# Performance work log

Measured on AMD Instinct MI355X. Metric: run time of the kernel, lower is better.

The kernel has to match this reference:

```python
import jax, jax.numpy as jnp
import numpy as np

N_NODES = 20000
N_EDGES = 320000
F_IN = 64      # num_node_features
C = 64         # out_features (per-head channels, concat=False)
H = 4          # n_heads
L = 3          # n_layers (stackable since F_IN == C)
N_RES = 2
N_PAIRS = 8192
EDGE_DIM = 9
HID = 64 * C   # ResNetGated hidden dim = 64 * out_features
N_EXPERTS = 8


def setup_inputs() -> dict:
    key = jax.random.key(0)
    ks = jax.random.split(key, 24)
    s = 0.05
    f32 = jnp.float32
    inp = {}
    inp["x"] = jax.random.normal(ks[0], (N_NODES, F_IN), f32)
    inp["edge_index"] = jax.random.randint(ks[1], (2, N_EDGES), 0, N_NODES)
    inp["edge_attr"] = jax.random.normal(ks[2], (N_EDGES, EDGE_DIM), f32)
    inp["edge_cross"] = jax.random.randint(ks[3], (N_PAIRS, 2), 0, N_NODES)
    inp["types"] = jax.random.randint(ks[4], (N_PAIRS,), 0, N_EXPERTS)
    # GATv2 encoder params, stacked over L layers (layer 0 in-dim == C)
    inp["gat_Wl"] = jax.random.normal(ks[5], (L, F_IN, H * C), f32) * s
    inp["gat_bl"] = jnp.full((L, H * C), 0.01, f32)
    inp["gat_Wr"] = jax.random.normal(ks[6], (L, F_IN, H * C), f32) * s
    inp["gat_br"] = jnp.full((L, H * C), 0.01, f32)
    inp["gat_We"] = jax.random.normal(ks[7], (L, EDGE_DIM, H * C), f32) * s  # lin_edge, no bias
    inp["gat_att"] = jax.random.normal(ks[8], (L, H, C), f32) * s
    inp["gat_bias"] = jnp.zeros((L, C), f32)
    inp["gat_gates"] = jax.random.normal(ks[9], (L,), f32) * 0.5
    # 8 type-routed experts: ResNetGated(2C -> 64C -> 2C) x N_RES, then Linear(2C, 1)
    inp["res_W1"] = jax.random.normal(ks[10], (N_EXPERTS, N_RES, 2 * C, HID), f32) * s
    inp["res_b1"] = jnp.full((N_EXPERTS, N_RES, HID), 0.01, f32)
    inp["res_W2"] = jax.random.normal(ks[11], (N_EXPERTS, N_RES, HID, 2 * C), f32) * s
    inp["res_b2"] = jnp.full((N_EXPERTS, N_RES, 2 * C), 0.01, f32)
    inp["res_gates"] = jax.random.normal(ks[12], (N_EXPERTS, N_RES), f32) * 0.5
    inp["head_W"] = jax.random.normal(ks[13], (N_EXPERTS, 2 * C, 1), f32) * s
    inp["head_b"] = jnp.full((N_EXPERTS, 1), 0.01, f32)
    return inp


def _gat_layer(h, src, tgt, ea, Wl, bl, Wr, br, We, att, bias):
    # GATv2Conv with edge features, concat=False (mean over heads)
    n = h.shape[0]
    nh, c = att.shape
    xl = (h @ Wl + bl).reshape(n, nh, c)   # source transform (x_j)
    xr = (h @ Wr + br).reshape(n, nh, c)   # target transform (x_i)
    e = (ea @ We).reshape(-1, nh, c)
    m = jax.nn.leaky_relu(xl[src] + xr[tgt] + e, 0.2)       # [E,H,C]
    logits = jnp.einsum('ehc,hc->eh', m, att)               # [E,H]
    mx = jax.ops.segment_max(logits, tgt, num_segments=n)
    a = jnp.exp(logits - mx[tgt])
    den = jax.ops.segment_sum(a, tgt, num_segments=n)
    alpha = a / den[tgt]                                     # segment softmax over in-edges
    out = jax.ops.segment_sum(xl[src] * alpha[:, :, None], tgt, num_segments=n)
    return out.mean(axis=1) + bias


def reference(x, edge_index, edge_attr, edge_cross, types,
              gat_Wl, gat_bl, gat_Wr, gat_br, gat_We, gat_att, gat_bias, gat_gates,
              res_W1, res_b1, res_W2, res_b2, res_gates, head_W, head_b):
    src, tgt = edge_index[0], edge_index[1]
    g = jax.nn.sigmoid(gat_gates)
    h = _gat_layer(x, src, tgt, edge_attr, gat_Wl[0], gat_bl[0], gat_Wr[0], gat_br[0],
                   gat_We[0], gat_att[0], gat_bias[0])
    for i in range(1, gat_Wl.shape[0]):
        h = jax.nn.leaky_relu(h, 0.01)
        hi = _gat_layer(h, src, tgt, edge_attr, gat_Wl[i], gat_bl[i], gat_Wr[i], gat_br[i],
                        gat_We[i], gat_att[i], gat_bias[i])
        h = g[i - 1] * hi + (1 - g[i - 1]) * h
    # pair gather + feature interleave: x[edge_cross].transpose(1,2).reshape(P, 2C)
    pair = h[edge_cross]                               # [P,2,C]
    p = pair.shape[0]
    z0 = jnp.swapaxes(pair, 1, 2).reshape(p, -1)        # [P,2C]
    outs = []
    for e in range(res_W1.shape[0]):
        z = z0
        ge = jax.nn.sigmoid(res_gates[e])
        for r in range(res_W1.shape[1]):
            z = jax.nn.relu(z)
            y = jax.nn.relu(z @ res_W1[e, r] + res_b1[e, r]) @ res_W2[e, r] + res_b2[e, r]
            z = ge[r] * y + (1 - ge[r]) * z
        outs.append(z @ head_W[e] + head_b[e])          # [P,1]
    all_out = jnp.stack(outs)                           # [8,P,1]
    per_row = all_out[types, jnp.arange(p)]             # [P,1] per-row expert output
    order = jnp.argsort(types, stable=True)             # concat groups type 0..7, stable in-group
    return per_row[order]
```

## Files before the change

kernel.cpp:

```cpp
#include <hip/hip_runtime.h>

#define NN 20000
#define NE 320000
#define NL 3
#define NP 8192
#define EDIM 9
#define TROWS 32
#define MAXT 272
#define CAPR (MAXT*TROWS)

typedef _Float16 f16x8 __attribute__((ext_vector_type(8)));
typedef float f32x4 __attribute__((ext_vector_type(4)));

#define GLL16(g,l) __builtin_amdgcn_global_load_lds((const __attribute__((address_space(1))) unsigned int*)(g), (__attribute__((address_space(3))) unsigned int*)(l), 16, 0, 0)

__device__ __forceinline__ float sigm(float x){ return 1.f/(1.f+__expf(-x)); }

__device__ __forceinline__ float dpp_sum64(float x){
  x += __int_as_float(__builtin_amdgcn_update_dpp(0, __float_as_int(x), 0x111, 0xf, 0xf, true));
  x += __int_as_float(__builtin_amdgcn_update_dpp(0, __float_as_int(x), 0x112, 0xf, 0xf, true));
  x += __int_as_float(__builtin_amdgcn_update_dpp(0, __float_as_int(x), 0x114, 0xf, 0xf, true));
  x += __int_as_float(__builtin_amdgcn_update_dpp(0, __float_as_int(x), 0x118, 0xf, 0xf, true));
  x += __int_as_float(__builtin_amdgcn_update_dpp(0, __float_as_int(x), 0x142, 0xf, 0xf, true));
  x += __int_as_float(__builtin_amdgcn_update_dpp(0, __float_as_int(x), 0x143, 0xf, 0xf, true));
  return __uint_as_float(__builtin_amdgcn_readlane(__float_as_uint(x), 63));
}

__global__ void k_fill_i(int* __restrict__ p, int n, int v){ int i=blockIdx.x*blockDim.x+threadIdx.x; if(i<n)p[i]=v; }

__global__ void k_deg(const int* __restrict__ ei, int* __restrict__ deg){
  int e=blockIdx.x*blockDim.x+threadIdx.x; if(e<NE) atomicAdd(&deg[ei[NE+e]],1);
}

__global__ __launch_bounds__(1024) void k_scan(const int* __restrict__ deg, int* __restrict__ row_ptr, int* __restrict__ cursor){
  __shared__ int sh[1024];
  __shared__ int carry;
  int tid=threadIdx.x;
  if(tid==0) carry=0;
  __syncthreads();
  for(int base=0;base<NN;base+=1024){
    int i=base+tid;
    int v=(i<NN)?deg[i]:0;
    sh[tid]=v; __syncthreads();
    for(int o=1;o<1024;o<<=1){
      int t=(tid>=o)?sh[tid-o]:0; __syncthreads();
      sh[tid]+=t; __syncthreads();
    }
    int incl=sh[tid];
    int c=carry;
    if(i<NN){ row_ptr[i+1]=c+incl; cursor[i]=c+incl-v; }
    if(i==0) row_ptr[0]=0;
    __syncthreads();
    if(tid==1023) carry=c+incl;
    __syncthreads();
  }
}

__global__ void k_fill_csr2(const int* __restrict__ ei, const float* __restrict__ ea,
    int* __restrict__ cursor, int* __restrict__ csr_src, float* __restrict__ eas){
  int e=blockIdx.x*blockDim.x+threadIdx.x;
  if(e<NE){
    int t=ei[NE+e]; int pos=atomicAdd(&cursor[t],1);
    csr_src[pos]=ei[e];
    const float* s=ea+(size_t)e*9;
    float* d=eas+(size_t)pos*12;
    #pragma unroll
    for(int k=0;k<9;++k) d[k]=s[k];
    d[9]=0.f; d[10]=0.f; d[11]=0.f;
  }
}

__global__ __launch_bounds__(256) void k_sort(const int* __restrict__ types, int* __restrict__ meta,
    int* __restrict__ slotp, int* __restrict__ islot){
  __shared__ int cnt[256][8];
  __shared__ int tot[8];
  __shared__ int base_s[8], pad_s[8];
  int tid=threadIdx.x;
  int lc[8]={0,0,0,0,0,0,0,0};
  int tl[32];
  for(int i=0;i<32;++i){ int ty=types[tid*32+i]; tl[i]=ty; lc[ty]++; }
  #pragma unroll
  for(int t=0;t<8;++t) cnt[tid][t]=lc[t];
  __syncthreads();
  if(tid<8){
    int run=0;
    for(int j=0;j<256;++j){ int v=cnt[j][tid]; cnt[j][tid]=run; run+=v; }
    tot[tid]=run;
  }
  __syncthreads();
  if(tid==0){
    int b=0, pb=0, nt=0;
    for(int t=0;t<8;++t){
      base_s[t]=b; pad_s[t]=pb;
      meta[t]=tot[t]; meta[8+t]=b; meta[16+t]=pb;
      int ntt=(tot[t]+31)>>5;
      for(int j=0;j<ntt;++j){ meta[32+nt]=t; meta[32+MAXT+nt]=pb+j*32; nt++; }
      b+=tot[t]; pb+=ntt*32;
    }
    meta[24]=nt; meta[25]=pb;
  }
  __syncthreads();
  if(tid<8){
    int t=tid; int ntt=(tot[t]+31)>>5;
    for(int sr=tot[t]; sr<ntt*32; ++sr) islot[pad_s[t]+sr]=-1;
  }
  int run[8];
  #pragma unroll
  for(int t=0;t<8;++t) run[t]=cnt[tid][t];
  for(int i=0;i<32;++i){
    int p=tid*32+i; int t=tl[i]; int r=run[t]++;
    int pos=base_s[t]+r, slot=pad_s[t]+r;
    slotp[p]=slot; islot[slot]=pos;
  }
}

__global__ __launch_bounds__(256) void k_nodexf(const float* __restrict__ hin,
    const float* __restrict__ Wl, const float* __restrict__ bl,
    const float* __restrict__ Wr, const float* __restrict__ br,
    float* __restrict__ xl, float* __restrict__ xr, int lk){
  __shared__ float hsT[64][68];
  __shared__ float ws[64][68];
  int bid=blockIdx.x;
  int n0=(bid>>3)*64, ch=bid&7;
  const float* W=(ch<4)?Wl:Wr;
  const float* bb=(ch<4)?bl:br;
  float* outp=(ch<4)?xl:xr;
  int c0=(ch&3)*64;
  int tid=threadIdx.x;

  for(int idx=tid; idx<64*16; idx+=256){
    int r=idx&63, kq=idx>>6;
    int n=n0+r;
    float4 v=make_float4(0.f,0.f,0.f,0.f);
    if(n<NN) v=*(const float4*)&hin[(size_t)n*64+kq*4];
    if(lk){
      v.x=v.x>0.f?v.x:0.01f*v.x; v.y=v.y>0.f?v.y:0.01f*v.y;
      v.z=v.z>0.f?v.z:0.01f*v.z; v.w=v.w>0.f?v.w:0.01f*v.w;
    }
    hsT[kq*4+0][r]=v.x; hsT[kq*4+1][r]=v.y; hsT[kq*4+2][r]=v.z; hsT[kq*4+3][r]=v.w;
  }
  for(int idx=tid; idx<64*16; idx+=256){
    int k=idx>>4, j4=idx&15;
    *(float4*)&ws[k][j4*4]=*(const float4*)&W[(size_t)k*256+c0+j4*4];
  }
  __syncthreads();

  int ty=tid>>4, tx=tid&15;
  float acc[4][4]={};
  #pragma unroll 4
  for(int k=0;k<64;++k){
    float4 a=*(const float4*)&hsT[k][4*ty];
    float4 b=*(const float4*)&ws[k][4*tx];
    float aa[4]={a.x,a.y,a.z,a.w}, bbv[4]={b.x,b.y,b.z,b.w};
    #pragma unroll
    for(int i=0;i<4;++i){
      #pragma unroll
      for(int j=0;j<4;++j) acc[i][j]=fmaf(aa[i],bbv[j],acc[i][j]);
    }
  }
  float4 bias4=*(const float4*)&bb[c0+4*tx];
  #pragma unroll
  for(int i=0;i<4;++i){
    int n=n0+4*ty+i;
    if(n<NN){
      float4 o=make_float4(acc[i][0]+bias4.x, acc[i][1]+bias4.y, acc[i][2]+bias4.z, acc[i][3]+bias4.w);
      *(float4*)&outp[(size_t)n*256+c0+4*tx]=o;
    }
  }
}

__global__ __launch_bounds__(256) void k_agg2(const float* __restrict__ xl, const float* __restrict__ xr,
    const float* __restrict__ eas, const int* __restrict__ csr_src, const int* __restrict__ row_ptr,
    const float* __restrict__ WeL, const float* __restrict__ attL,
    const float* __restrict__ biasL, const float* __restrict__ gates, int layer,
    const float* __restrict__ hprev, float* __restrict__ hout){
  __shared__ float red[4][64];
  int n=blockIdx.x, tid=threadIdx.x;
  float w0=WeL[tid],      w1=WeL[256+tid],  w2=WeL[512+tid],  w3=WeL[768+tid],  w4=WeL[1024+tid];
  float w5=WeL[1280+tid], w6=WeL[1536+tid], w7=WeL[1792+tid], w8=WeL[2048+tid];
  float att_t=attL[tid];
  float xr_t=xr[(size_t)n*256+tid];
  int s=row_ptr[n], t=row_ptr[n+1];
  float den=0.f, acc=0.f;

  auto body=[&](float xlv, int j){
    const float4* ep=(const float4*)(eas+(size_t)j*12);
    float4 e0=ep[0], e1=ep[1];
    float e8=eas[(size_t)j*12+8];
    float ev=e0.x*w0+e0.y*w1+e0.z*w2+e0.w*w3+e1.x*w4+e1.y*w5+e1.z*w6+e1.w*w7+e8*w8;
    float m=xlv+xr_t+ev;
    m=m>0.f?m:0.2f*m;
    float pt=dpp_sum64(m*att_t);
    float a=__expf(pt);
    den+=a; acc+=a*xlv;
  };

  float x0=0.f,x1=0.f,x2=0.f,x3=0.f;
  if(s+0<t) x0=xl[(size_t)csr_src[s+0]*256+tid];
  if(s+1<t) x1=xl[(size_t)csr_src[s+1]*256+tid];
  if(s+2<t) x2=xl[(size_t)csr_src[s+2]*256+tid];
  if(s+3<t) x3=xl[(size_t)csr_src[s+3]*256+tid];
  int j=s;
  while(j+7<t){
    float y0=xl[(size_t)csr_src[j+4]*256+tid];
    float y1=xl[(size_t)csr_src[j+5]*256+tid];
    float y2=xl[(size_t)csr_src[j+6]*256+tid];
    float y3=xl[(size_t)csr_src[j+7]*256+tid];
    body(x0,j); body(x1,j+1); body(x2,j+2); body(x3,j+3);
    x0=y0; x1=y1; x2=y2; x3=y3;
    j+=4;
  }
  if(j<t){ body(x0,j); ++j; }
  if(j<t){ body(x1,j); ++j; }
  if(j<t){ body(x2,j); ++j; }
  if(j<t){ body(x3,j); ++j; }
  while(j<t){ body(xl[(size_t)csr_src[j]*256+tid], j); ++j; }

  float rdn=den>0.f?1.f/den:0.f;
  int h=tid>>6, cc=tid&63;
  red[h][cc]=acc*rdn;
  __syncthreads();
  if(tid<64){
    float mean=(red[0][tid]+red[1][tid]+red[2][tid]+red[3][tid])*0.25f + biasL[tid];
    float o;
    if(layer==0) o=mean;
    else{
      float hp=hprev[(size_t)n*64+tid];
      hp=hp>0.f?hp:0.01f*hp;
      float g=sigm(gates[layer-1]);
      o=g*mean+(1.f-g)*hp;
    }
    hout[(size_t)n*64+tid]=o;
  }
}

__global__ void k_buildz(const float* __restrict__ hfin, const int* __restrict__ ecross,
    const int* __restrict__ slotp, float* __restrict__ z){
  int g=blockIdx.x*blockDim.x+threadIdx.x;
  if(g>=NP*64) return;
  int p=g>>6, c=g&63;
  int a=ecross[2*p], b=ecross[2*p+1];
  int slot=slotp[p];
  float2 v; v.x=hfin[(size_t)a*64+c]; v.y=hfin[(size_t)b*64+c];
  ((float2*)(z+(size_t)slot*128))[c]=v;
}

__global__ __launch_bounds__(256) void k_prepw1(const float* __restrict__ src, _Float16* __restrict__ dst){
  __shared__ float lds[128][33];
  int bid=blockIdx.x, er=bid>>7, ch=bid&127;
  const float* s=src+(size_t)er*128*4096 + ch*32;
  int tid=threadIdx.x;
  for(int idx=tid; idx<128*32; idx+=256){ int k=idx>>5, jl=idx&31; lds[k][jl]=s[(size_t)k*4096+jl]; }
  __syncthreads();
  _Float16* d=dst+(size_t)bid*4096;
  for(int g=tid; g<512; g+=256){
    int jl=g>>4, k8=g&15;
    f16x8 v;
    #pragma unroll
    for(int t=0;t<8;++t) v[t]=(_Float16)lds[k8*8+t][jl];
    int elem=(jl*128+k8*8)^((jl&7)<<3);
    *(f16x8*)(&d[elem])=v;
  }
}

__global__ __launch_bounds__(256) void k_prepw2(const float* __restrict__ src, _Float16* __restrict__ dst){
  __shared__ float lds[32][130];
  int bid=blockIdx.x, er=bid>>7, ch=bid&127;
  const float* s=src+(size_t)er*4096*128 + (size_t)ch*32*128;
  int tid=threadIdx.x;
  for(int idx=tid; idx<32*128; idx+=256){ int j=idx>>7, n=idx&127; lds[j][n]=s[(size_t)j*128+n]; }
  __syncthreads();
  _Float16* d=dst+(size_t)bid*4096;
  for(int g=tid; g<512; g+=256){
    int n=g>>2, j8=g&3;
    f16x8 v;
    #pragma unroll
    for(int t=0;t<8;++t) v[t]=(_Float16)lds[j8*8+t][n];
    int elem=(n*32+j8*8)^((n&7)<<3);
    *(f16x8*)(&d[elem])=v;
  }
}

__global__ __launch_bounds__(256) void k_resmfma(const float* __restrict__ zin,
    const _Float16* __restrict__ w1t, const _Float16* __restrict__ w2t,
    const float* __restrict__ b1all, const int* __restrict__ meta,
    float* __restrict__ ypart, int rb)
{
  __shared__ _Float16 zh[32*128];
  __shared__ _Float16 wb[2][8192];
  __shared__ _Float16 ts[32*32];
  __shared__ float b1s[1024];
  int bidl=blockIdx.x;
  int bid=(bidl&7)*132+(bidl>>3);
  int v=bid>>2, hq=bid&3;
  int nt=meta[24];
  if(v>=nt) return;
  int e=meta[32+v], row0=meta[32+MAXT+v];
  int er=e*2+rb;
  const _Float16* w1b=w1t+(size_t)er*524288 + (size_t)hq*32*4096;
  const _Float16* w2b=w2t+(size_t)er*524288 + (size_t)hq*32*4096;
  const float* b1g=b1all+(size_t)er*4096 + hq*1024;
  int tid=threadIdx.x, l=tid&63, w=tid>>6;
  int lm=l&15, lq=l>>4;
  int s16=(w&1)*16, jh=w>>1;
  int arow=s16+lm;

  for(int g=tid; g<512; g+=256){
    int row=g>>4, slot=g&15;
    const float* src=zin+(size_t)(row0+row)*128+slot*8;
    float4 v0=*(const float4*)src;
    float4 v1=*(const float4*)(src+4);
    f16x8 hv;
    hv[0]=(_Float16)fmaxf(v0.x,0.f); hv[1]=(_Float16)fmaxf(v0.y,0.f);
    hv[2]=(_Float16)fmaxf(v0.z,0.f); hv[3]=(_Float16)fmaxf(v0.w,0.f);
    hv[4]=(_Float16)fmaxf(v1.x,0.f); hv[5]=(_Float16)fmaxf(v1.y,0.f);
    hv[6]=(_Float16)fmaxf(v1.z,0.f); hv[7]=(_Float16)fmaxf(v1.w,0.f);
    *(f16x8*)(&zh[(row*128+slot*8)^((row&7)<<3)])=hv;
  }
  for(int g=tid; g<1024; g+=256) b1s[g]=b1g[g];

  #pragma unroll
  for(int s=0;s<2;++s){
    int so=(w*2+s)*512;
    GLL16(w1b+so+l*8, &wb[0][so]);
    GLL16(w2b+so+l*8, &wb[0][4096+so]);
  }
  asm volatile("s_waitcnt lgkmcnt(0)" ::: "memory");
  __builtin_amdgcn_sched_barrier(0);
  __builtin_amdgcn_s_barrier();

  f32x4 yacc[4];
  #pragma unroll
  for(int i=0;i<4;++i){ yacc[i][0]=0.f; yacc[i][1]=0.f; yacc[i][2]=0.f; yacc[i][3]=0.f; }

  for(int cc=0; cc<32; ++cc){
    int buf=cc&1;
    if(cc<31){
      const _Float16* g1=w1b+(size_t)(cc+1)*4096;
      const _Float16* g2=w2b+(size_t)(cc+1)*4096;
      int nb=buf^1;
      #pragma unroll
      for(int s=0;s<2;++s){
        int so=(w*2+s)*512;
        GLL16(g1+so+l*8, &wb[nb][so]);
        GLL16(g2+so+l*8, &wb[nb][4096+so]);
      }
      asm volatile("s_waitcnt vmcnt(4)" ::: "memory");
    }else{
      asm volatile("s_waitcnt vmcnt(0)" ::: "memory");
    }
    __builtin_amdgcn_sched_barrier(0);
    __builtin_amdgcn_s_barrier();

    f32x4 tacc={0.f,0.f,0.f,0.f};
    int j=jh*16+lm;
    #pragma unroll
    for(int ks=0;ks<4;++ks){
      f16x8 a=*(const f16x8*)(&zh[(arow*128+ks*32+lq*8)^((arow&7)<<3)]);
      f16x8 b=*(const f16x8*)(&wb[buf][(j*128+ks*32+lq*8)^((j&7)<<3)]);
      tacc=__builtin_amdgcn_mfma_f32_16x16x32_f16(a,b,tacc,0,0,0);
    }
    float b1v=b1s[cc*32+j];
    #pragma unroll
    for(int r=0;r<4;++r){
      int trow=s16+lq*4+r;
      ts[(trow*32+j)^((trow&7)<<3)]=(_Float16)fmaxf(tacc[r]+b1v,0.f);
    }
    asm volatile("s_waitcnt lgkmcnt(0)" ::: "memory");
    __builtin_amdgcn_sched_barrier(0);
    __builtin_amdgcn_s_barrier();

    f16x8 a2=*(const f16x8*)(&ts[(arow*32+lq*8)^((arow&7)<<3)]);
    #pragma unroll
    for(int nf=0;nf<4;++nf){
      int n=jh*64+nf*16+lm;
      f16x8 b=*(const f16x8*)(&wb[buf][4096+((n*32+lq*8)^((n&7)<<3))]);
      yacc[nf]=__builtin_amdgcn_mfma_f32_16x16x32_f16(a2,b,yacc[nf],0,0,0);
    }
    __builtin_amdgcn_s_barrier();
  }

  float* yp=ypart+(size_t)hq*CAPR*128;
  #pragma unroll
  for(int nf=0;nf<4;++nf){
    int col=jh*64+nf*16+lm;
    #pragma unroll
    for(int r=0;r<4;++r)
      yp[(size_t)(row0+s16+lq*4+r)*128+col]=yacc[nf][r];
  }
}

__global__ __launch_bounds__(256) void k_comb(const float* __restrict__ zin, const float* __restrict__ ypart,
    const float* __restrict__ b2all, const float* __restrict__ gates, const int* __restrict__ meta,
    int rb, float* __restrict__ zout,
    const float* __restrict__ hWg, const float* __restrict__ hbg, const int* __restrict__ islot,
    float* __restrict__ out)
{
  int v=blockIdx.x;
  if(v>=meta[24]) return;
  int e=meta[32+v], row0=meta[32+MAXT+v];
  int er=e*2+rb;
  float ge=sigm(gates[er]);
  const float* b2=b2all+(size_t)er*128;
  int tid=threadIdx.x;
  const size_t HS=(size_t)CAPR*128;
  if(rb==0){
    for(int idx=tid; idx<32*128; idx+=256){
      int r=idx>>7, c=idx&127;
      size_t o=(size_t)(row0+r)*128+c;
      float y=ypart[o]+ypart[HS+o]+ypart[2*HS+o]+ypart[3*HS+o];
      float zr=fmaxf(zin[o],0.f);
      zout[o]=ge*(y+b2[c])+(1.f-ge)*zr;
    }
  }else{
    int r=tid>>3, cs=tid&7;
    float acc=0.f;
    size_t ro=(size_t)(row0+r)*128;
    #pragma unroll
    for(int q=0;q<16;++q){
      int c=cs*16+q;
      size_t o=ro+c;
      float y=ypart[o]+ypart[HS+o]+ypart[2*HS+o]+ypart[3*HS+o];
      float zr=fmaxf(zin[o],0.f);
      float zf=ge*(y+b2[c])+(1.f-ge)*zr;
      acc+=zf*hWg[e*128+c];
    }
    acc+=__shfl_xor(acc,1); acc+=__shfl_xor(acc,2); acc+=__shfl_xor(acc,4);
    if(cs==0){
      int pos=islot[row0+r];
      if(pos>=0) out[pos]=acc+hbg[e];
    }
  }
}

extern "C" void kernel_launch(void* const* d_in, const int* in_sizes, int n_in,
                              void* d_out, int out_size, void* d_ws, size_t ws_size,
                              hipStream_t stream){
  const float* x     =(const float*)d_in[0];
  const int*   ei    =(const int*)  d_in[1];
  const float* ea    =(const float*)d_in[2];
  const int*   ecross=(const int*)  d_in[3];
  const int*   types =(const int*)  d_in[4];
  const float* gWl   =(const float*)d_in[5];
  const float* gbl   =(const float*)d_in[6];
  const float* gWr   =(const float*)d_in[7];
  const float* gbr   =(const float*)d_in[8];
  const float* gWe   =(const float*)d_in[9];
  const float* gatt  =(const float*)d_in[10];
  const float* gbias =(const float*)d_in[11];
  const float* ggate =(const float*)d_in[12];
  const float* rW1   =(const float*)d_in[13];
  const float* rb1   =(const float*)d_in[14];
  const float* rW2   =(const float*)d_in[15];
  const float* rb2   =(const float*)d_in[16];
  const float* rg    =(const float*)d_in[17];
  const float* hW    =(const float*)d_in[18];
  const float* hb    =(const float*)d_in[19];
  float* out=(float*)d_out;

  char* base=(char*)d_ws;
  size_t off=0;
  auto alloc=[&](size_t bytes)->char*{
    char* p=base+off;
    off=(off+bytes+511)&~((size_t)511);
    return p;
  };
  float* hA     =(float*)alloc((size_t)NN*64*4);
  float* hB     =(float*)alloc((size_t)NN*64*4);
  int*   deg    =(int*)  alloc((size_t)NN*4);
  int*   row_ptr=(int*)  alloc((size_t)(NN+1)*4);
  int*   cursor =(int*)  alloc((size_t)NN*4);
  int*   csr_src=(int*)  alloc((size_t)(NE+16)*4);
  int*   meta   =(int*)  alloc(1024*4);
  int*   slotp  =(int*)  alloc((size_t)NP*4);
  int*   islot  =(int*)  alloc((size_t)CAPR*4);
  float* zA     =(float*)alloc((size_t)CAPR*128*4);
  size_t uoff=off;
  float* xl =(float*)(base+uoff);
  float* xr =(float*)(base+uoff+(size_t)NN*256*4);
  float* eas=(float*)(base+uoff+(size_t)NN*256*4*2);
  _Float16* w1t=(_Float16*)(base+uoff);
  _Float16* w2t=(_Float16*)(base+uoff+(size_t)16*524288*2);
  float* ypart =(float*)(base+uoff+(size_t)16*524288*2*2);
  size_t gat_bytes=(size_t)NN*256*4*2 + (size_t)(NE*12+16)*4;
  size_t exp_bytes=(size_t)16*524288*2*2 + (size_t)4*CAPR*128*4;
  size_t need=uoff+(gat_bytes>exp_bytes?gat_bytes:exp_bytes);
  if(ws_size<need) return;
  float* zB=hB;

  k_fill_i<<<(NN+255)/256,256,0,stream>>>(deg,NN,0);
  k_deg<<<(NE+255)/256,256,0,stream>>>(ei,deg);
  k_scan<<<1,1024,0,stream>>>(deg,row_ptr,cursor);
  k_fill_csr2<<<(NE+255)/256,256,0,stream>>>(ei,ea,cursor,csr_src,eas);
  k_sort<<<1,256,0,stream>>>(types,meta,slotp,islot);

  const float* hcur=x;
  float* hnext=hA;
  for(int L=0;L<NL;++L){
    k_nodexf<<<((NN+63)/64)*8,256,0,stream>>>(hcur, gWl+(size_t)L*64*256, gbl+(size_t)L*256,
                                              gWr+(size_t)L*64*256, gbr+(size_t)L*256, xl, xr, L>0?1:0);
    k_agg2<<<NN,256,0,stream>>>(xl,xr,eas,csr_src,row_ptr, gWe+(size_t)L*EDIM*256,
                                gatt+(size_t)L*256, gbias+(size_t)L*64, ggate, L, hcur, hnext);
    hcur=hnext;
    hnext=(hcur==hA)?hB:hA;
  }

  k_buildz<<<NP*64/256,256,0,stream>>>(hcur,ecross,slotp,zA);

  k_prepw1<<<2048,256,0,stream>>>(rW1,w1t);
  k_prepw2<<<2048,256,0,stream>>>(rW2,w2t);

  k_resmfma<<<1056,256,0,stream>>>(zA,w1t,w2t,rb1,meta,ypart,0);
  k_comb<<<MAXT,256,0,stream>>>(zA,ypart,rb2,rg,meta,0,zB,hW,hb,islot,out);
  k_resmfma<<<1056,256,0,stream>>>(zB,w1t,w2t,rb1,meta,ypart,1);
  k_comb<<<MAXT,256,0,stream>>>(zB,ypart,rb2,rg,meta,1,zA,hW,hb,islot,out);

  (void)in_sizes; (void)n_in; (void)out_size;
}
```

Baseline: 582.0 us.

## Parallelize CSR prefix scan, deepen aggregation gather prefetch, use exp2 softmax

Replaces the single-block serial prefix scan over node degrees with a three-kernel multi-block scan: per-block scan, serial block-offset pass, then add-back. In the GAT aggregation kernel, the xl gather prefetch window doubles from 4 to 8 edges to hide more gather latency. The attention logit is pre-scaled by log2(e) so exp2f can replace __expf, and leaky-ReLU becomes fmaxf. It adds two kernel launches and more live registers in the aggregation loop, which may lower occupancy.

```diff
diff --git a/kernel.cpp b/kernel.cpp
--- a/kernel.cpp
+++ b/kernel.cpp
@@ -8,6 +8,7 @@
 #define TROWS 32
 #define MAXT 272
 #define CAPR (MAXT*TROWS)
+#define NB ((NN+255)/256)
 
 typedef _Float16 f16x8 __attribute__((ext_vector_type(8)));
 typedef float f32x4 __attribute__((ext_vector_type(4)));
@@ -32,28 +33,33 @@
   int e=blockIdx.x*blockDim.x+threadIdx.x; if(e<NE) atomicAdd(&deg[ei[NE+e]],1);
 }
 
-__global__ __launch_bounds__(1024) void k_scan(const int* __restrict__ deg, int* __restrict__ row_ptr, int* __restrict__ cursor){
-  __shared__ int sh[1024];
-  __shared__ int carry;
-  int tid=threadIdx.x;
-  if(tid==0) carry=0;
-  __syncthreads();
-  for(int base=0;base<NN;base+=1024){
-    int i=base+tid;
-    int v=(i<NN)?deg[i]:0;
-    sh[tid]=v; __syncthreads();
-    for(int o=1;o<1024;o<<=1){
-      int t=(tid>=o)?sh[tid-o]:0; __syncthreads();
-      sh[tid]+=t; __syncthreads();
-    }
-    int incl=sh[tid];
-    int c=carry;
-    if(i<NN){ row_ptr[i+1]=c+incl; cursor[i]=c+incl-v; }
-    if(i==0) row_ptr[0]=0;
-    __syncthreads();
-    if(tid==1023) carry=c+incl;
-    __syncthreads();
-  }
+__global__ __launch_bounds__(256) void k_scan1(const int* __restrict__ deg, int* __restrict__ incl, int* __restrict__ bsum){
+  __shared__ int sh[256];
+  int b=blockIdx.x, tid=threadIdx.x;
+  int i=b*256+tid;
+  int v=(i<NN)?deg[i]:0;
+  sh[tid]=v; __syncthreads();
+  for(int o=1;o<256;o<<=1){
+    int t=(tid>=o)?sh[tid-o]:0; __syncthreads();
+    sh[tid]+=t; __syncthreads();
+  }
+  if(i<NN) incl[i]=sh[tid];
+  if(tid==255) bsum[b]=sh[255];
+}
+__global__ void k_scan2(const int* __restrict__ bsum, int* __restrict__ boff){
+  if(blockIdx.x==0 && threadIdx.x==0){
+    int run=0;
+    for(int b=0;b<NB;++b){ boff[b]=run; run+=bsum[b]; }
+  }
+}
+__global__ void k_scan3(const int* __restrict__ deg, const int* __restrict__ incl,
+                        const int* __restrict__ boff, int* __restrict__ row_ptr, int* __restrict__ cursor){
+  int i=blockIdx.x*blockDim.x+threadIdx.x;
+  if(i<NN){
+    int r=incl[i]+boff[i>>8];
+    row_ptr[i+1]=r; cursor[i]=r-deg[i];
+  }
+  if(i==0) row_ptr[0]=0;
 }
 
 __global__ void k_fill_csr2(const int* __restrict__ ei, const float* __restrict__ ea,
@@ -178,7 +184,7 @@
   int n=blockIdx.x, tid=threadIdx.x;
   float w0=WeL[tid],      w1=WeL[256+tid],  w2=WeL[512+tid],  w3=WeL[768+tid],  w4=WeL[1024+tid];
   float w5=WeL[1280+tid], w6=WeL[1536+tid], w7=WeL[1792+tid], w8=WeL[2048+tid];
-  float att_t=attL[tid];
+  float att_t=attL[tid]*1.44269504089f;
   float xr_t=xr[(size_t)n*256+tid];
   int s=row_ptr[n], t=row_ptr[n+1];
   float den=0.f, acc=0.f;
@@ -189,31 +195,40 @@
     float e8=eas[(size_t)j*12+8];
     float ev=e0.x*w0+e0.y*w1+e0.z*w2+e0.w*w3+e1.x*w4+e1.y*w5+e1.z*w6+e1.w*w7+e8*w8;
     float m=xlv+xr_t+ev;
-    m=m>0.f?m:0.2f*m;
+    m=fmaxf(m,0.2f*m);
     float pt=dpp_sum64(m*att_t);
-    float a=__expf(pt);
+    float a=exp2f(pt);
     den+=a; acc+=a*xlv;
   };
 
-  float x0=0.f,x1=0.f,x2=0.f,x3=0.f;
+  float x0=0.f,x1=0.f,x2=0.f,x3=0.f,x4=0.f,x5=0.f,x6=0.f,x7=0.f;
   if(s+0<t) x0=xl[(size_t)csr_src[s+0]*256+tid];
   if(s+1<t) x1=xl[(size_t)csr_src[s+1]*256+tid];
   if(s+2<t) x2=xl[(size_t)csr_src[s+2]*256+tid];
   if(s+3<t) x3=xl[(size_t)csr_src[s+3]*256+tid];
+  if(s+4<t) x4=xl[(size_t)csr_src[s+4]*256+tid];
+  if(s+5<t) x5=xl[(size_t)csr_src[s+5]*256+tid];
+  if(s+6<t) x6=xl[(size_t)csr_src[s+6]*256+tid];
+  if(s+7<t) x7=xl[(size_t)csr_src[s+7]*256+tid];
   int j=s;
-  while(j+7<t){
-    float y0=xl[(size_t)csr_src[j+4]*256+tid];
-    float y1=xl[(size_t)csr_src[j+5]*256+tid];
-    float y2=xl[(size_t)csr_src[j+6]*256+tid];
-    float y3=xl[(size_t)csr_src[j+7]*256+tid];
+  while(j+11<t){
+    float y0=xl[(size_t)csr_src[j+8]*256+tid];
+    float y1=xl[(size_t)csr_src[j+9]*256+tid];
+    float y2=xl[(size_t)csr_src[j+10]*256+tid];
+    float y3=xl[(size_t)csr_src[j+11]*256+tid];
     body(x0,j); body(x1,j+1); body(x2,j+2); body(x3,j+3);
-    x0=y0; x1=y1; x2=y2; x3=y3;
+    x0=x4; x1=x5; x2=x6; x3=x7;
+    x4=y0; x5=y1; x6=y2; x7=y3;
     j+=4;
   }
   if(j<t){ body(x0,j); ++j; }
   if(j<t){ body(x1,j); ++j; }
   if(j<t){ body(x2,j); ++j; }
   if(j<t){ body(x3,j); ++j; }
+  if(j<t){ body(x4,j); ++j; }
+  if(j<t){ body(x5,j); ++j; }
+  if(j<t){ body(x6,j); ++j; }
+  if(j<t){ body(x7,j); ++j; }
   while(j<t){ body(xl[(size_t)csr_src[j]*256+tid], j); ++j; }
 
   float rdn=den>0.f?1.f/den:0.f;
@@ -470,6 +485,9 @@
   int*   deg    =(int*)  alloc((size_t)NN*4);
   int*   row_ptr=(int*)  alloc((size_t)(NN+1)*4);
   int*   cursor =(int*)  alloc((size_t)NN*4);
+  int*   incl   =(int*)  alloc((size_t)NN*4);
+  int*   bsum   =(int*)  alloc(256*4);
+  int*   boff   =(int*)  alloc(256*4);
   int*   csr_src=(int*)  alloc((size_t)(NE+16)*4);
   int*   meta   =(int*)  alloc(1024*4);
   int*   slotp  =(int*)  alloc((size_t)NP*4);
@@ -490,7 +508,9 @@
 
   k_fill_i<<<(NN+255)/256,256,0,stream>>>(deg,NN,0);
   k_deg<<<(NE+255)/256,256,0,stream>>>(ei,deg);
-  k_scan<<<1,1024,0,stream>>>(deg,row_ptr,cursor);
+  k_scan1<<<NB,256,0,stream>>>(deg,incl,bsum);
+  k_scan2<<<1,64,0,stream>>>(bsum,boff);
+  k_scan3<<<(NN+255)/256,256,0,stream>>>(deg,incl,boff,row_ptr,cursor);
   k_fill_csr2<<<(NE+255)/256,256,0,stream>>>(ei,ea,cursor,csr_src,eas);
   k_sort<<<1,256,0,stream>>>(types,meta,slotp,islot);
 
```

Measured after the change: 578.6 us. About the same (-0.6%).
